# Kernel tuning notes

Measured on AMD Instinct MI355X. Metric: run time of the kernel, lower is better.

Reference implementation:

```python
import jax, jax.numpy as jnp
import numpy as np

B, C, H, W = 4, 256, 64, 64
PD = 32  # projection_dim = in_channels // projection_ratio


def setup_inputs() -> dict:
    key = jax.random.key(0)
    ks = jax.random.split(key, 7)
    x = jax.random.normal(ks[0], (B, C, H, W), dtype=jnp.float32)
    Wq = jax.random.normal(ks[1], (PD, C), dtype=jnp.float32) * (1.0 / np.sqrt(C))
    bq = jax.random.normal(ks[2], (PD,), dtype=jnp.float32) * 0.01
    Wk = jax.random.normal(ks[3], (PD, C), dtype=jnp.float32) * (1.0 / np.sqrt(C))
    bk = jax.random.normal(ks[4], (PD,), dtype=jnp.float32) * 0.01
    Wv = jax.random.normal(ks[5], (C, C), dtype=jnp.float32) * (1.0 / np.sqrt(C))
    bv = jax.random.normal(ks[6], (C,), dtype=jnp.float32) * 0.01
    gamma = jnp.float32(1.0)
    return {"x": x, "Wq": Wq, "bq": bq, "Wk": Wk, "bk": bk, "Wv": Wv, "bv": bv, "gamma": gamma}


def reference(x, Wq, bq, Wk, bk, Wv, bv, gamma):
    b, c, h, w = x.shape
    xf = x.reshape(b, c, h * w)                      # [B, C, N]
    q = jnp.einsum('dc,bcn->bnd', Wq, xf) + bq       # [B, N, PD]
    k = jnp.einsum('dc,bcn->bdn', Wk, xf) + bk[:, None]   # [B, PD, N]
    v = jnp.einsum('ec,bcn->ben', Wv, xf) + bv[:, None]   # [B, C, N]
    scores = jnp.einsum('bnd,bdm->bnm', q, k)        # [B, N, N] (no scaling, per original)
    attn = jax.nn.softmax(scores, axis=-1)           # softmax over keys
    out = jnp.einsum('bcn,bmn->bcm', v, attn)        # v @ attn^T -> [B, C, N]
    out = out.reshape(b, c, h, w)
    return gamma * out + x
```

## Files before the change

### kernel.cpp

```cpp
#include <hip/hip_runtime.h>
#include <stdint.h>

typedef _Float16 half_t;
typedef __attribute__((ext_vector_type(8))) _Float16 f16x8;
typedef __attribute__((ext_vector_type(4))) _Float16 f16x4;
typedef __attribute__((ext_vector_type(2))) __fp16 fp16x2;
typedef __attribute__((ext_vector_type(4))) float f32x4;
typedef __attribute__((ext_vector_type(16))) float f32x16;
typedef __attribute__((ext_vector_type(4))) uint32_t u32x4;
typedef __attribute__((ext_vector_type(2))) int i32x2;

#define DEVI __device__ __forceinline__

static constexpr int Bn = 4, Cc = 256, Nn = 4096, PD = 32;
static constexpr float L2E = 1.44269504089f;

__device__ half_t g_Q[(size_t)Bn * Nn * PD];
__device__ half_t g_K[(size_t)Bn * Nn * PD];
__device__ half_t g_V[(size_t)Bn * Cc * Nn];

DEVI f16x8 cvt8(float4 a, float4 b) {
    f16x8 r;
    r[0] = (_Float16)a.x; r[1] = (_Float16)a.y; r[2] = (_Float16)a.z; r[3] = (_Float16)a.w;
    r[4] = (_Float16)b.x; r[5] = (_Float16)b.y; r[6] = (_Float16)b.z; r[7] = (_Float16)b.w;
    return r;
}

DEVI uint32_t pkrtz(float a, float b) {
    fp16x2 h = __builtin_amdgcn_cvt_pkrtz(a, b);
    return __builtin_bit_cast(uint32_t, h);
}

DEVI float asf(int u) { return __builtin_bit_cast(float, u); }
DEVI int   asi(float f) { return __builtin_bit_cast(int, f); }

DEVI i32x2 pl32swap(int a, int b) {
    return __builtin_amdgcn_permlane32_swap(a, b, false, false);
}

DEVI void gll16(const void* g, void* l) {
    auto gp = (const __attribute__((address_space(1))) uint32_t*)(uintptr_t)g;
    auto lp = (__attribute__((address_space(3))) uint32_t*)(uintptr_t)l;
    __builtin_amdgcn_global_load_lds(gp, lp, 16, 0, 0);
}

__global__ __launch_bounds__(256, 1) void proj_kernel(
    const float* __restrict__ x,
    const float* __restrict__ Wq, const float* __restrict__ bq,
    const float* __restrict__ Wk, const float* __restrict__ bk,
    const float* __restrict__ Wv, const float* __restrict__ bv)
{
    __shared__ __align__(16) half_t xt[64 * 40];

    const int b    = blockIdx.x >> 6;
    const int n0   = (blockIdx.x & 63) * 64;
    const int t    = threadIdx.x;
    const int w    = t >> 6;
    const int lane = t & 63;
    const int l15  = lane & 15, g = lane >> 4;

    f32x4 qk_acc[4] = {};
    f32x4 v_acc[4][4] = {};

    const float* wrow_qk = (w < 2) ? (Wq + (size_t)(16 * w + l15) * Cc)
                                   : (Wk + (size_t)(16 * (w - 2) + l15) * Cc);

    for (int cs = 0; cs < 8; ++cs) {
        const int c0 = cs * 32;
        {
            const int nl = t & 63;
            const int cg = t >> 6;
            const float* xp = x + ((size_t)(b * Cc + c0 + cg * 8)) * Nn + n0 + nl;
            float f[8];
#pragma unroll
            for (int q = 0; q < 8; ++q) f[q] = xp[(size_t)q * Nn];
            f16x4 h0, h1;
#pragma unroll
            for (int q = 0; q < 4; ++q) { h0[q] = (_Float16)f[q]; h1[q] = (_Float16)f[q + 4]; }
            *(f16x4*)&xt[nl * 40 + cg * 8]     = h0;
            *(f16x4*)&xt[nl * 40 + cg * 8 + 4] = h1;
        }
        __syncthreads();

        f16x8 xf[4];
#pragma unroll
        for (int nf = 0; nf < 4; ++nf)
            xf[nf] = *(const f16x8*)&xt[(nf * 16 + l15) * 40 + g * 8];

        {
            const float* wp = wrow_qk + c0 + g * 8;
            const f16x8 af = cvt8(*(const float4*)wp, *(const float4*)(wp + 4));
#pragma unroll
            for (int nt = 0; nt < 4; ++nt)
                qk_acc[nt] = __builtin_amdgcn_mfma_f32_16x16x32_f16(af, xf[nt], qk_acc[nt], 0, 0, 0);
        }
#pragma unroll
        for (int et = 0; et < 4; ++et) {
            const int e = (w * 4 + et) * 16 + l15;
            const float* wp = Wv + (size_t)e * Cc + c0 + g * 8;
            const f16x8 wf = cvt8(*(const float4*)wp, *(const float4*)(wp + 4));
#pragma unroll
            for (int nf = 0; nf < 4; ++nf)
                v_acc[et][nf] = __builtin_amdgcn_mfma_f32_16x16x32_f16(xf[nf], wf, v_acc[et][nf], 0, 0, 0);
        }
        __syncthreads();
    }

    {
        const float* bias = (w < 2) ? bq : bk;
        const int dbase = 16 * (w & 1) + 4 * g;
        float bb[4];
#pragma unroll
        for (int r = 0; r < 4; ++r) bb[r] = bias[dbase + r];
        half_t* dst = (w < 2) ? g_Q : g_K;
#pragma unroll
        for (int nt = 0; nt < 4; ++nt) {
            const int n = n0 + nt * 16 + l15;
            f16x4 h;
#pragma unroll
            for (int r = 0; r < 4; ++r) h[r] = (_Float16)(qk_acc[nt][r] + bb[r]);
            *(f16x4*)&dst[((size_t)b * Nn + n) * PD + dbase] = h;
        }
    }
#pragma unroll
    for (int et = 0; et < 4; ++et) {
        const int e = (w * 4 + et) * 16 + l15;
        const float bve = bv[e];
#pragma unroll
        for (int nf = 0; nf < 4; ++nf) {
            const int n = n0 + nf * 16 + 4 * g;
            f16x4 h;
#pragma unroll
            for (int r = 0; r < 4; ++r) h[r] = (_Float16)(v_acc[et][nf][r] + bve);
            *(f16x4*)&g_V[((size_t)b * Cc + e) * Nn + n] = h;
        }
    }
}

__global__ __launch_bounds__(256, 2) void attn_kernel(
    const float* __restrict__ x, const float* __restrict__ gamma_p, float* __restrict__ out)
{
    __shared__ __align__(16) half_t V_lds[2][128 * 64];
    __shared__ float mrg[2][64][36];
    __shared__ float mx[2][2][32];
    __shared__ float lx[2][2][32];

    const int blk = blockIdx.x;
    const int grp = blk & 7;
    const int mt  = blk >> 3;
    const int b   = grp >> 1;
    const int eh  = grp & 1;
    const int e0  = eh * 128;

    const int t    = threadIdx.x;
    const int w    = t >> 6;
    const int lane = t & 63;
    const int l31  = lane & 31;
    const int hi   = lane >> 5;
    const int mh   = w >> 1, kk = w & 1;
    const int mrow0 = mt * 64 + mh * 32;

    const half_t* Kb  = g_K + (size_t)b * Nn * PD;
    const half_t* Vbg = g_V + (size_t)b * Cc * Nn;

    const half_t* qp = g_Q + ((size_t)b * Nn + mrow0 + l31) * PD + hi * 8;
    const f16x8 q0 = *(const f16x8*)qp;
    const f16x8 q1 = *(const f16x8*)(qp + 16);

    const int vrow = lane >> 3;
    const int vcol = (((lane & 7) ^ vrow) * 8);
    const half_t* vptr[4];
#pragma unroll
    for (int ch = 0; ch < 4; ++ch)
        vptr[ch] = Vbg + (size_t)(e0 + w * 32 + ch * 8 + vrow) * Nn + vcol;

    const int e7   = l31 & 7;
    const int off0 = (((kk * 4) + hi) ^ e7) * 8;
    const int off1 = (((kk * 4) + 2 + hi) ^ e7) * 8;

    f32x16 acc[4] = {};
    float run_m = -1e30f, run_l = 0.f;
    const f32x16 zero16 = {};

    f32x16 s;
    f16x8 kq0, kq1;

    {
        const half_t* kp0 = Kb + (size_t)(kk * 32 + l31) * PD + hi * 8;
        const f16x8 ka = *(const f16x8*)kp0;
        const f16x8 kb = *(const f16x8*)(kp0 + 16);
        s = __builtin_amdgcn_mfma_f32_32x32x16_f16(ka, q0, zero16, 0, 0, 0);
        s = __builtin_amdgcn_mfma_f32_32x32x16_f16(kb, q1, s, 0, 0, 0);
    }
#pragma unroll
    for (int ch = 0; ch < 4; ++ch)
        gll16(vptr[ch], &V_lds[0][(w * 32 + ch * 8) * 64]);
    __builtin_amdgcn_sched_barrier(0);
    const half_t* kp = Kb + (size_t)(64 + kk * 32 + l31) * PD + hi * 8;
    kq0 = *(const f16x8*)kp;
    kq1 = *(const f16x8*)(kp + 16);
    __builtin_amdgcn_sched_barrier(0);

    constexpr int NT = Nn / 64;
    for (int i = 0; i < NT; ++i) {
        const int buf = i & 1;
        const bool more = (i + 1 < NT);

        asm volatile("s_waitcnt vmcnt(2)" ::: "memory");
        __builtin_amdgcn_s_barrier();
        __builtin_amdgcn_sched_barrier(0);

        float tm = s[0];
#pragma unroll
        for (int r = 1; r < 16; ++r) tm = fmaxf(tm, s[r]);
        {
            const i32x2 rr = pl32swap(asi(tm), asi(tm));
            tm = fmaxf(asf(rr[0]), asf(rr[1]));
        }
        float alpha = 1.f;
        if (__any(tm > run_m + 8.f)) {
            const float nm = fmaxf(run_m, tm);
            alpha = __builtin_amdgcn_exp2f((run_m - nm) * L2E);
            run_m = nm;
            float a16[16];
#pragma unroll
            for (int r = 0; r < 16; ++r)
                a16[r] = __shfl(alpha, (r & 3) + 8 * (r >> 2) + 4 * hi);
#pragma unroll
            for (int et = 0; et < 4; ++et)
#pragma unroll
                for (int r = 0; r < 16; ++r) acc[et][r] *= a16[r];
        }

        const float nms = run_m * L2E;
        float p[16];
#pragma unroll
        for (int r = 0; r < 16; ++r)
            p[r] = __builtin_amdgcn_exp2f(s[r] * L2E - nms);
        float rs = (((p[0] + p[1]) + (p[2] + p[3])) + ((p[4] + p[5]) + (p[6] + p[7])))
                 + (((p[8] + p[9]) + (p[10] + p[11])) + ((p[12] + p[13]) + (p[14] + p[15])));
        {
            const i32x2 rr = pl32swap(asi(rs), asi(rs));
            rs = asf(rr[0]) + asf(rr[1]);
        }
        run_l = run_l * alpha + rs;

        f16x8 pa0, pa1;
        {
            const i32x2 r0 = pl32swap((int)pkrtz(p[0], p[1]), (int)pkrtz(p[4], p[5]));
            const i32x2 r1 = pl32swap((int)pkrtz(p[2], p[3]), (int)pkrtz(p[6], p[7]));
            u32x4 d0 = {(uint32_t)r0[0], (uint32_t)r1[0], (uint32_t)r0[1], (uint32_t)r1[1]};
            pa0 = __builtin_bit_cast(f16x8, d0);
            const i32x2 r2 = pl32swap((int)pkrtz(p[8], p[9]),   (int)pkrtz(p[12], p[13]));
            const i32x2 r3 = pl32swap((int)pkrtz(p[10], p[11]), (int)pkrtz(p[14], p[15]));
            u32x4 d1 = {(uint32_t)r2[0], (uint32_t)r3[0], (uint32_t)r2[1], (uint32_t)r3[1]};
            pa1 = __builtin_bit_cast(f16x8, d1);
        }

        if (more) {
#pragma unroll
            for (int ch = 0; ch < 4; ++ch) {
                vptr[ch] += 64;
                gll16(vptr[ch], &V_lds[buf ^ 1][(w * 32 + ch * 8) * 64]);
            }
        }
        __builtin_amdgcn_sched_barrier(0);

        __builtin_amdgcn_s_setprio(1);
#pragma unroll
        for (int et = 0; et < 4; ++et) {
            const int rowb = (et * 32 + l31) * 64;
            const f16x8 vf0 = *(const f16x8*)&V_lds[buf][rowb + off0];
            const f16x8 vf1 = *(const f16x8*)&V_lds[buf][rowb + off1];
            acc[et] = __builtin_amdgcn_mfma_f32_32x32x16_f16(pa0, vf0, acc[et], 0, 0, 0);
            acc[et] = __builtin_amdgcn_mfma_f32_32x32x16_f16(pa1, vf1, acc[et], 0, 0, 0);
        }
        __builtin_amdgcn_s_setprio(0);

        if (more) {
            s = __builtin_amdgcn_mfma_f32_32x32x16_f16(kq0, q0, zero16, 0, 0, 0);
            s = __builtin_amdgcn_mfma_f32_32x32x16_f16(kq1, q1, s, 0, 0, 0);
            kp += 64 * PD;
            if (i + 2 >= NT) kp = Kb + (size_t)(kk * 32 + l31) * PD + hi * 8;
            kq0 = *(const f16x8*)kp;
            kq1 = *(const f16x8*)(kp + 16);
            __builtin_amdgcn_sched_barrier(0);
        }
    }

    if (lane < 32) { mx[kk][mh][l31] = run_m; lx[kk][mh][l31] = run_l; }
    __syncthreads();

    const float mo = mx[kk ^ 1][mh][l31];
    const float lo = lx[kk ^ 1][mh][l31];
    const float M  = fmaxf(run_m, mo);
    const float ssf = __builtin_amdgcn_exp2f((run_m - M) * L2E);
    const float sof = __builtin_amdgcn_exp2f((mo - M) * L2E);
    const float inv = 1.0f / (run_l * ssf + lo * sof);
    float sc16[16], li16[16];
#pragma unroll
    for (int r = 0; r < 16; ++r) {
        const int src = (r & 3) + 8 * (r >> 2) + 4 * hi;
        sc16[r] = __shfl(ssf, src);
        li16[r] = __shfl(inv, src);
    }

    const float gm = gamma_p[0];
#pragma unroll
    for (int h = 0; h < 2; ++h) {
        __syncthreads();
        if (kk == 1) {
#pragma unroll
            for (int e2 = 0; e2 < 2; ++e2) {
                const int et  = 2 * h + e2;
                const int ell = e2 * 32 + l31;
#pragma unroll
                for (int q = 0; q < 4; ++q) {
                    float4 v;
                    v.x = acc[et][4 * q + 0] * sc16[4 * q + 0];
                    v.y = acc[et][4 * q + 1] * sc16[4 * q + 1];
                    v.z = acc[et][4 * q + 2] * sc16[4 * q + 2];
                    v.w = acc[et][4 * q + 3] * sc16[4 * q + 3];
                    *(float4*)&mrg[mh][ell][8 * q + 4 * hi] = v;
                }
            }
        }
        __syncthreads();
        if (kk == 0) {
#pragma unroll
            for (int e2 = 0; e2 < 2; ++e2) {
                const int et  = 2 * h + e2;
                const int ell = e2 * 32 + l31;
                const int e   = e0 + et * 32 + l31;
#pragma unroll
                for (int q = 0; q < 4; ++q) {
                    const float4 part = *(const float4*)&mrg[mh][ell][8 * q + 4 * hi];
                    const size_t idx = ((size_t)b * Cc + e) * Nn + mrow0 + 8 * q + 4 * hi;
                    const float4 xin = *(const float4*)&x[idx];
                    float4 o;
                    o.x = gm * (acc[et][4 * q + 0] * sc16[4 * q + 0] + part.x) * li16[4 * q + 0] + xin.x;
                    o.y = gm * (acc[et][4 * q + 1] * sc16[4 * q + 1] + part.y) * li16[4 * q + 1] + xin.y;
                    o.z = gm * (acc[et][4 * q + 2] * sc16[4 * q + 2] + part.z) * li16[4 * q + 2] + xin.z;
                    o.w = gm * (acc[et][4 * q + 3] * sc16[4 * q + 3] + part.w) * li16[4 * q + 3] + xin.w;
                    *(float4*)&out[idx] = o;
                }
            }
        }
    }
}

extern "C" void kernel_launch(void* const* d_in, const int* in_sizes, int n_in,
                              void* d_out, int out_size, void* d_ws, size_t ws_size,
                              hipStream_t stream) {
    (void)in_sizes; (void)n_in; (void)out_size; (void)d_ws; (void)ws_size;
    const float* x  = (const float*)d_in[0];
    const float* Wq = (const float*)d_in[1];
    const float* bq = (const float*)d_in[2];
    const float* Wk = (const float*)d_in[3];
    const float* bk = (const float*)d_in[4];
    const float* Wv = (const float*)d_in[5];
    const float* bv = (const float*)d_in[6];
    const float* gm = (const float*)d_in[7];
    float* out = (float*)d_out;

    proj_kernel<<<256, 256, 0, stream>>>(x, Wq, bq, Wk, bk, Wv, bv);
    attn_kernel<<<512, 256, 0, stream>>>(x, gm, out);
}
```

Baseline: 93.34 us.

## Cover all 256 channels per block with a 4-way key split and 512 threads

The attention kernel now uses 512-thread blocks, each handling all 256 value channels for 64 query rows. The key dimension is split four ways across warps, with 128 keys per iteration. Previously two blocks each recomputed QK^T and softmax for half the channels, so this removes that duplicated score and exp work and halves the grid. In exchange each thread holds twice the accumulators (8 f32x16 tiles), LDS use grows to 128 KB with the V buffer reused for a 4-way merge, and register pressure and occupancy may suffer.

```diff
diff --git a/kernel.cpp b/kernel.cpp
--- a/kernel.cpp
+++ b/kernel.cpp
@@ -137,27 +137,25 @@
     }
 }
 
-__global__ __launch_bounds__(256, 2) void attn_kernel(
+__global__ __launch_bounds__(512, 2) void attn_kernel(
     const float* __restrict__ x, const float* __restrict__ gamma_p, float* __restrict__ out)
 {
-    __shared__ __align__(16) half_t V_lds[2][128 * 64];
-    __shared__ float mrg[2][64][36];
-    __shared__ float mx[2][2][32];
-    __shared__ float lx[2][2][32];
+    __shared__ __align__(16) half_t V_lds[2][256 * 128];
+    __shared__ float mx[2][4][32];
+    __shared__ float lx[2][4][32];
 
     const int blk = blockIdx.x;
     const int grp = blk & 7;
-    const int mt  = blk >> 3;
     const int b   = grp >> 1;
-    const int eh  = grp & 1;
-    const int e0  = eh * 128;
+    const int mt  = ((blk >> 3) << 1) | (grp & 1);
 
     const int t    = threadIdx.x;
     const int w    = t >> 6;
     const int lane = t & 63;
     const int l31  = lane & 31;
     const int hi   = lane >> 5;
-    const int mh   = w >> 1, kk = w & 1;
+    const int kk   = w & 3;
+    const int mh   = w >> 2;
     const int mrow0 = mt * 64 + mh * 32;
 
     const half_t* Kb  = g_K + (size_t)b * Nn * PD;
@@ -167,18 +165,14 @@
     const f16x8 q0 = *(const f16x8*)qp;
     const f16x8 q1 = *(const f16x8*)(qp + 16);
 
-    const int vrow = lane >> 3;
-    const int vcol = (((lane & 7) ^ vrow) * 8);
-    const half_t* vptr[4];
-#pragma unroll
-    for (int ch = 0; ch < 4; ++ch)
-        vptr[ch] = Vbg + (size_t)(e0 + w * 32 + ch * 8 + vrow) * Nn + vcol;
+    const int vr = w * 4 + (lane >> 4);
+    const half_t* vb = Vbg + (size_t)vr * Nn + (((lane & 15) ^ (vr & 7)) * 8);
 
     const int e7   = l31 & 7;
     const int off0 = (((kk * 4) + hi) ^ e7) * 8;
     const int off1 = (((kk * 4) + 2 + hi) ^ e7) * 8;
 
-    f32x16 acc[4] = {};
+    f32x16 acc[8] = {};
     float run_m = -1e30f, run_l = 0.f;
     const f32x16 zero16 = {};
 
@@ -193,15 +187,15 @@
         s = __builtin_amdgcn_mfma_f32_32x32x16_f16(kb, q1, s, 0, 0, 0);
     }
 #pragma unroll
-    for (int ch = 0; ch < 4; ++ch)
-        gll16(vptr[ch], &V_lds[0][(w * 32 + ch * 8) * 64]);
+    for (int rr = 0; rr < 8; ++rr)
+        gll16(vb + (size_t)rr * 32 * Nn, &V_lds[0][rr * 4096 + w * 512]);
     __builtin_amdgcn_sched_barrier(0);
-    const half_t* kp = Kb + (size_t)(64 + kk * 32 + l31) * PD + hi * 8;
+    const half_t* kp = Kb + (size_t)(128 + kk * 32 + l31) * PD + hi * 8;
     kq0 = *(const f16x8*)kp;
     kq1 = *(const f16x8*)(kp + 16);
     __builtin_amdgcn_sched_barrier(0);
 
-    constexpr int NT = Nn / 64;
+    constexpr int NT = Nn / 128;
     for (int i = 0; i < NT; ++i) {
         const int buf = i & 1;
         const bool more = (i + 1 < NT);
@@ -227,7 +221,7 @@
             for (int r = 0; r < 16; ++r)
                 a16[r] = __shfl(alpha, (r & 3) + 8 * (r >> 2) + 4 * hi);
 #pragma unroll
-            for (int et = 0; et < 4; ++et)
+            for (int et = 0; et < 8; ++et)
 #pragma unroll
                 for (int r = 0; r < 16; ++r) acc[et][r] *= a16[r];
         }
@@ -259,17 +253,16 @@
 
         if (more) {
 #pragma unroll
-            for (int ch = 0; ch < 4; ++ch) {
-                vptr[ch] += 64;
-                gll16(vptr[ch], &V_lds[buf ^ 1][(w * 32 + ch * 8) * 64]);
-            }
+            for (int rr = 0; rr < 8; ++rr)
+                gll16(vb + 128 + (size_t)rr * 32 * Nn, &V_lds[buf ^ 1][rr * 4096 + w * 512]);
+            vb += 128;
         }
         __builtin_amdgcn_sched_barrier(0);
 
         __builtin_amdgcn_s_setprio(1);
 #pragma unroll
-        for (int et = 0; et < 4; ++et) {
-            const int rowb = (et * 32 + l31) * 64;
+        for (int et = 0; et < 8; ++et) {
+            const int rowb = (et * 32 + l31) * 128;
             const f16x8 vf0 = *(const f16x8*)&V_lds[buf][rowb + off0];
             const f16x8 vf1 = *(const f16x8*)&V_lds[buf][rowb + off1];
             acc[et] = __builtin_amdgcn_mfma_f32_32x32x16_f16(pa0, vf0, acc[et], 0, 0, 0);
@@ -280,7 +273,7 @@
         if (more) {
             s = __builtin_amdgcn_mfma_f32_32x32x16_f16(kq0, q0, zero16, 0, 0, 0);
             s = __builtin_amdgcn_mfma_f32_32x32x16_f16(kq1, q1, s, 0, 0, 0);
-            kp += 64 * PD;
+            kp += 128 * PD;
             if (i + 2 >= NT) kp = Kb + (size_t)(kk * 32 + l31) * PD + hi * 8;
             kq0 = *(const f16x8*)kp;
             kq1 = *(const f16x8*)(kp + 16);
@@ -288,64 +281,67 @@
         }
     }
 
-    if (lane < 32) { mx[kk][mh][l31] = run_m; lx[kk][mh][l31] = run_l; }
+    if (lane < 32) { mx[mh][kk][l31] = run_m; lx[mh][kk][l31] = run_l; }
     __syncthreads();
 
-    const float mo = mx[kk ^ 1][mh][l31];
-    const float lo = lx[kk ^ 1][mh][l31];
-    const float M  = fmaxf(run_m, mo);
-    const float ssf = __builtin_amdgcn_exp2f((run_m - M) * L2E);
-    const float sof = __builtin_amdgcn_exp2f((mo - M) * L2E);
-    const float inv = 1.0f / (run_l * ssf + lo * sof);
     float sc16[16], li16[16];
-#pragma unroll
-    for (int r = 0; r < 16; ++r) {
-        const int src = (r & 3) + 8 * (r >> 2) + 4 * hi;
-        sc16[r] = __shfl(ssf, src);
-        li16[r] = __shfl(inv, src);
-    }
+    {
+        const float m0 = mx[mh][0][l31], m1 = mx[mh][1][l31];
+        const float m2 = mx[mh][2][l31], m3 = mx[mh][3][l31];
+        const float M  = fmaxf(fmaxf(m0, m1), fmaxf(m2, m3));
+        const float L  = lx[mh][0][l31] * __builtin_amdgcn_exp2f((m0 - M) * L2E)
+                       + lx[mh][1][l31] * __builtin_amdgcn_exp2f((m1 - M) * L2E)
+                       + lx[mh][2][l31] * __builtin_amdgcn_exp2f((m2 - M) * L2E)
+                       + lx[mh][3][l31] * __builtin_amdgcn_exp2f((m3 - M) * L2E);
+        const float ssf = __builtin_amdgcn_exp2f((run_m - M) * L2E);
+        const float inv = 1.0f / L;
+#pragma unroll
+        for (int r = 0; r < 16; ++r) {
+            const int src = (r & 3) + 8 * (r >> 2) + 4 * hi;
+            sc16[r] = __shfl(ssf, src);
+            li16[r] = __shfl(inv, src);
+        }
+    }
+    __syncthreads();
 
     const float gm = gamma_p[0];
+    float4* mrg = (float4*)&V_lds[0][0];
 #pragma unroll
     for (int h = 0; h < 2; ++h) {
+#pragma unroll
+        for (int j = 0; j < 4; ++j) {
+            const int et = h * 4 + j;
+#pragma unroll
+            for (int q = 0; q < 4; ++q) {
+                float4 v;
+                v.x = acc[et][4 * q + 0] * sc16[4 * q + 0];
+                v.y = acc[et][4 * q + 1] * sc16[4 * q + 1];
+                v.z = acc[et][4 * q + 2] * sc16[4 * q + 2];
+                v.w = acc[et][4 * q + 3] * sc16[4 * q + 3];
+                mrg[((w * 4 + j) * 4 + q) * 64 + lane] = v;
+            }
+        }
         __syncthreads();
-        if (kk == 1) {
-#pragma unroll
-            for (int e2 = 0; e2 < 2; ++e2) {
-                const int et  = 2 * h + e2;
-                const int ell = e2 * 32 + l31;
-#pragma unroll
-                for (int q = 0; q < 4; ++q) {
-                    float4 v;
-                    v.x = acc[et][4 * q + 0] * sc16[4 * q + 0];
-                    v.y = acc[et][4 * q + 1] * sc16[4 * q + 1];
-                    v.z = acc[et][4 * q + 2] * sc16[4 * q + 2];
-                    v.w = acc[et][4 * q + 3] * sc16[4 * q + 3];
-                    *(float4*)&mrg[mh][ell][8 * q + 4 * hi] = v;
-                }
+        {
+            const int et = h * 4 + kk;
+            const int e  = et * 32 + l31;
+#pragma unroll
+            for (int q = 0; q < 4; ++q) {
+                float4 s0 = mrg[(((mh * 4 + 0) * 4 + kk) * 4 + q) * 64 + lane];
+                float4 s1 = mrg[(((mh * 4 + 1) * 4 + kk) * 4 + q) * 64 + lane];
+                float4 s2 = mrg[(((mh * 4 + 2) * 4 + kk) * 4 + q) * 64 + lane];
+                float4 s3 = mrg[(((mh * 4 + 3) * 4 + kk) * 4 + q) * 64 + lane];
+                const size_t idx = ((size_t)b * Cc + e) * Nn + mrow0 + 8 * q + 4 * hi;
+                const float4 xin = *(const float4*)&x[idx];
+                float4 o;
+                o.x = gm * (s0.x + s1.x + s2.x + s3.x) * li16[4 * q + 0] + xin.x;
+                o.y = gm * (s0.y + s1.y + s2.y + s3.y) * li16[4 * q + 1] + xin.y;
+                o.z = gm * (s0.z + s1.z + s2.z + s3.z) * li16[4 * q + 2] + xin.z;
+                o.w = gm * (s0.w + s1.w + s2.w + s3.w) * li16[4 * q + 3] + xin.w;
+                *(float4*)&out[idx] = o;
             }
         }
         __syncthreads();
-        if (kk == 0) {
-#pragma unroll
-            for (int e2 = 0; e2 < 2; ++e2) {
-                const int et  = 2 * h + e2;
-                const int ell = e2 * 32 + l31;
-                const int e   = e0 + et * 32 + l31;
-#pragma unroll
-                for (int q = 0; q < 4; ++q) {
-                    const float4 part = *(const float4*)&mrg[mh][ell][8 * q + 4 * hi];
-                    const size_t idx = ((size_t)b * Cc + e) * Nn + mrow0 + 8 * q + 4 * hi;
-                    const float4 xin = *(const float4*)&x[idx];
-                    float4 o;
-                    o.x = gm * (acc[et][4 * q + 0] * sc16[4 * q + 0] + part.x) * li16[4 * q + 0] + xin.x;
-                    o.y = gm * (acc[et][4 * q + 1] * sc16[4 * q + 1] + part.y) * li16[4 * q + 1] + xin.y;
-                    o.z = gm * (acc[et][4 * q + 2] * sc16[4 * q + 2] + part.z) * li16[4 * q + 2] + xin.z;
-                    o.w = gm * (acc[et][4 * q + 3] * sc16[4 * q + 3] + part.w) * li16[4 * q + 3] + xin.w;
-                    *(float4*)&out[idx] = o;
-                }
-            }
-        }
     }
 }
 
@@ -364,5 +360,5 @@
     float* out = (float*)d_out;
 
     proj_kernel<<<256, 256, 0, stream>>>(x, Wq, bq, Wk, bk, Wv, bv);
-    attn_kernel<<<512, 256, 0, stream>>>(x, gm, out);
-}
+    attn_kernel<<<256, 512, 0, stream>>>(x, gm, out);
+}
```

Measured after the change: 81.34 us. 12.9% less time.
